# Kernel optimization log

Hardware: AMD Instinct MI355X
Metric: run time of the kernel (lower is better)

The kernel has to match this reference:

```python
import jax, jax.numpy as jnp
import numpy as np

EPS = 1e-5

def _layernorm(x, g, b):
    mu = jnp.mean(x, axis=-1, keepdims=True)
    var = jnp.mean(jnp.square(x - mu), axis=-1, keepdims=True)
    return (x - mu) * jax.lax.rsqrt(var + EPS) * g + b

def setup_inputs() -> dict:
    key = jax.random.key(0)
    ks = jax.random.split(key, 8)
    B, T, D, H = 2, 2048, 1024, 16
    hd = D // H
    s = 0.02
    return {
        "x": jax.random.normal(ks[0], (B, T, D), jnp.float32),
        "wq": jax.random.normal(ks[1], (H, D, hd), jnp.float32) * s,
        "wk": jax.random.normal(ks[2], (H, D, hd), jnp.float32) * s,
        "wv": jax.random.normal(ks[3], (H, D, hd), jnp.float32) * s,
        "w_proj": jax.random.normal(ks[4], (D, D), jnp.float32) * s,
        "b_proj": jnp.zeros((D,), jnp.float32),
        "w_ff1": jax.random.normal(ks[5], (D, 4 * D), jnp.float32) * s,
        "b_ff1": jnp.zeros((4 * D,), jnp.float32),
        "w_ff2": jax.random.normal(ks[6], (4 * D, D), jnp.float32) * s,
        "b_ff2": jnp.zeros((D,), jnp.float32),
        "ln1_g": jnp.ones((D,), jnp.float32),
        "ln1_b": jnp.zeros((D,), jnp.float32),
        "ln2_g": jnp.ones((D,), jnp.float32),
        "ln2_b": jnp.zeros((D,), jnp.float32),
    }

def reference(x, wq, wk, wv, w_proj, b_proj, w_ff1, b_ff1, w_ff2, b_ff2,
              ln1_g, ln1_b, ln2_g, ln2_b):
    B, T, D = x.shape
    H, _, hd = wq.shape
    # --- self-attention sublayer (pre-LN) ---
    h = _layernorm(x, ln1_g, ln1_b)
    # per-head Q/K/V projections batched over heads (math identical to per-head linears)
    q = jnp.einsum('btd,hds->bhts', h, wq)
    k = jnp.einsum('btd,hds->bhts', h, wk)
    v = jnp.einsum('btd,hds->bhts', h, wv)
    att = jnp.einsum('bhts,bhTs->bhtT', q, k) * (hd ** -0.5)  # [B,H,T,T]
    causal = jnp.tril(jnp.ones((T, T), dtype=bool))
    att = jnp.where(causal, att, jnp.float32(-jnp.inf))
    att = jax.nn.softmax(att, axis=-1)
    o = jnp.einsum('bhtT,bhTs->bhts', att, v)                 # [B,H,T,hd]
    o = o.transpose(0, 2, 1, 3).reshape(B, T, H * hd)         # concat heads
    x = x + o @ w_proj + b_proj
    # --- FFN sublayer (pre-LN) ---
    h2 = _layernorm(x, ln2_g, ln2_b)
    ff = jax.nn.relu(h2 @ w_ff1 + b_ff1) @ w_ff2 + b_ff2
    return x + ff
```

## Files before the change

### kernel.cpp

```cpp
#include <hip/hip_runtime.h>

typedef unsigned short u16;
typedef unsigned int   u32;
typedef __bf16 bf16;
typedef bf16 bf16x8 __attribute__((ext_vector_type(8)));
typedef float f32x4 __attribute__((ext_vector_type(4)));
typedef u32 u32x4 __attribute__((ext_vector_type(4)));

__device__ inline u16 f2bf(float f) {
  union { float f; u32 u; } cv; cv.f = f;
  u32 u = cv.u;
  return (u16)((u + 0x7FFFu + ((u >> 16) & 1u)) >> 16);
}

__device__ __forceinline__ void gld16(const void* g, void* l) {
  __builtin_amdgcn_global_load_lds(
      (const __attribute__((address_space(1))) void*)g,
      (__attribute__((address_space(3))) void*)l, 16, 0, 0);
}

template<bool ADDB>
__global__ __launch_bounds__(256) void ln_kernel(
    const float* __restrict__ x, const float* __restrict__ g,
    const float* __restrict__ b, u16* __restrict__ out,
    const float* __restrict__ badd, float* __restrict__ xwb)
{
  const int row = blockIdx.x;
  const int t = threadIdx.x;
  const float4 v = *reinterpret_cast<const float4*>(&x[(size_t)row*1024 + t*4]);
  float s  = v.x + v.y + v.z + v.w;
  float sq = v.x*v.x + v.y*v.y + v.z*v.z + v.w*v.w;
  #pragma unroll
  for (int off = 32; off; off >>= 1) { s += __shfl_down(s, off); sq += __shfl_down(sq, off); }
  __shared__ float red[8];
  const int wave = t >> 6, lane = t & 63;
  if (lane == 0) { red[wave] = s; red[wave + 4] = sq; }
  __syncthreads();
  __shared__ float stats[2];
  if (t == 0) {
    float S  = red[0] + red[1] + red[2] + red[3];
    float SQ = red[4] + red[5] + red[6] + red[7];
    float mu = S * (1.0f/1024.0f);
    float var = SQ * (1.0f/1024.0f) - mu*mu;
    stats[0] = mu; stats[1] = rsqrtf(var + 1e-5f);
  }
  __syncthreads();
  const float mu = stats[0], rv = stats[1];
  const float4 gv = *reinterpret_cast<const float4*>(&g[t*4]);
  const float4 bv = *reinterpret_cast<const float4*>(&b[t*4]);
  u16 o4[4];
  o4[0] = f2bf((v.x - mu)*rv*gv.x + bv.x);
  o4[1] = f2bf((v.y - mu)*rv*gv.y + bv.y);
  o4[2] = f2bf((v.z - mu)*rv*gv.z + bv.z);
  o4[3] = f2bf((v.w - mu)*rv*gv.w + bv.w);
  u32 p0 = (u32)o4[0] | ((u32)o4[1] << 16);
  u32 p1 = (u32)o4[2] | ((u32)o4[3] << 16);
  u32* op = reinterpret_cast<u32*>(&out[(size_t)row*1024 + t*4]);
  op[0] = p0; op[1] = p1;
  if (ADDB) {
    const float4 av = *reinterpret_cast<const float4*>(&badd[t*4]);
    float4 w;
    w.x = v.x + av.x; w.y = v.y + av.y; w.z = v.z + av.z; w.w = v.w + av.w;
    *reinterpret_cast<float4*>(&xwb[(size_t)row*1024 + t*4]) = w;
  }
}

__global__ __launch_bounds__(256) void transpose_cast(
    const float* __restrict__ in, u16* __restrict__ out, int R, int C)
{
  __shared__ float tile[32][33];
  const int tx = threadIdx.x, ty = threadIdx.y;
  const size_t bo = (size_t)blockIdx.z * R * C;
  const int r0 = blockIdx.y * 32, c0 = blockIdx.x * 32;
  #pragma unroll
  for (int j = 0; j < 4; ++j)
    tile[ty + j*8][tx] = in[bo + (size_t)(r0 + ty + j*8)*C + c0 + tx];
  __syncthreads();
  #pragma unroll
  for (int j = 0; j < 4; ++j)
    out[bo + (size_t)(c0 + ty + j*8)*R + r0 + tx] = f2bf(tile[tx][ty + j*8]);
}

__global__ __launch_bounds__(256) void vt_kernel(
    const u16* __restrict__ qkv, u16* __restrict__ vt, int T)
{
  __shared__ u16 tile[32][33];
  const int tx = threadIdx.x, ty = threadIdx.y;
  const int bh = blockIdx.z, b = bh >> 4, h = bh & 15;
  const int r0 = blockIdx.x * 32;
  const int c0 = blockIdx.y * 32;
  const size_t tokbase = (size_t)b * T;
  #pragma unroll
  for (int j = 0; j < 4; ++j)
    tile[ty + j*8][tx] = qkv[(tokbase + r0 + ty + j*8)*3072 + 2048 + h*64 + c0 + tx];
  __syncthreads();
  #pragma unroll
  for (int j = 0; j < 4; ++j)
    vt[((size_t)bh*64 + c0 + ty + j*8)*T + r0 + tx] = tile[tx][ty + j*8];
}

__global__ __launch_bounds__(512, 2) void gemm_128(
    const u16* __restrict__ A, const u16* __restrict__ BT,
    int M, int N, int K,
    const float* __restrict__ bias, const float* __restrict__ resid,
    float* __restrict__ Cout)
{
  __shared__ __align__(16) u16 Alds[2][128*64];
  __shared__ __align__(16) u16 Blds[2][128*64];
  const int t = threadIdx.x;
  const int wave = t >> 6, lane = t & 63;
  const int wm = wave >> 2, wn = wave & 3;
  const int g = lane >> 4, r = lane & 15;
  const int m0 = blockIdx.y * 128, n0 = blockIdx.x * 128;
  const int NTk = K >> 6;

  f32x4 acc[4][2] = {};

  auto STAGE = [&](int buf, int kt) {
    const int k0 = kt << 6;
    #pragma unroll
    for (int p = 0; p < 2; ++p) {
      const int c = t + p*512;
      const int row = c >> 3;
      const int col = (((c & 7) ^ (row & 7)) << 3);
      gld16(&A[(size_t)(m0 + row)*K + k0 + col], &Alds[buf][c*8]);
    }
    #pragma unroll
    for (int p = 0; p < 2; ++p) {
      const int c = t + p*512;
      const int row = c >> 3;
      const int col = (((c & 7) ^ (row & 7)) << 3);
      gld16(&BT[(size_t)(n0 + row)*K + k0 + col], &Blds[buf][c*8]);
    }
  };

  STAGE(0, 0);
  if (NTk > 1) STAGE(1, 1);

  const int csw = (r & 7) << 3;

  for (int kt = 0; kt < NTk; ++kt) {
    const int buf = kt & 1;
    if (kt + 1 < NTk) asm volatile("s_waitcnt vmcnt(4)" ::: "memory");
    else              asm volatile("s_waitcnt vmcnt(0)" ::: "memory");
    __builtin_amdgcn_s_barrier();
    #pragma unroll
    for (int ks = 0; ks < 2; ++ks) {
      bf16x8 af[4], bfr[2];
      #pragma unroll
      for (int i = 0; i < 4; ++i)
        af[i] = *reinterpret_cast<const bf16x8*>(
            &Alds[buf][(wm*64 + i*16 + r)*64 + ((ks*32 + g*8) ^ csw)]);
      #pragma unroll
      for (int j = 0; j < 2; ++j)
        bfr[j] = *reinterpret_cast<const bf16x8*>(
            &Blds[buf][(wn*32 + j*16 + r)*64 + ((ks*32 + g*8) ^ csw)]);
      __builtin_amdgcn_s_setprio(1);
      #pragma unroll
      for (int i = 0; i < 4; ++i)
        #pragma unroll
        for (int j = 0; j < 2; ++j)
          acc[i][j] = __builtin_amdgcn_mfma_f32_16x16x32_bf16(af[i], bfr[j], acc[i][j], 0, 0, 0);
      __builtin_amdgcn_s_setprio(0);
    }
    __builtin_amdgcn_s_barrier();
    if (kt + 2 < NTk) STAGE(buf, kt + 2);
  }

  #pragma unroll
  for (int mi = 0; mi < 4; ++mi) {
    #pragma unroll
    for (int ni = 0; ni < 2; ++ni) {
      #pragma unroll
      for (int i = 0; i < 4; ++i) {
        const int gm = m0 + wm*64 + mi*16 + g*4 + i;
        const int gn = n0 + wn*32 + ni*16 + r;
        const size_t idx = (size_t)gm * N + gn;
        Cout[idx] = acc[mi][ni][i] + bias[gn] + resid[idx];
      }
    }
  }
}

__global__ __launch_bounds__(512, 2) void gemm_128_sk(
    const u16* __restrict__ A, const u16* __restrict__ BT,
    int M, int N, int K, float* __restrict__ Cout)
{
  __shared__ __align__(16) u16 Alds[2][128*64];
  __shared__ __align__(16) u16 Blds[2][128*64];
  const int bid = blockIdx.x;
  const int s = bid >> 3;
  const int n0 = (s & 7) * 128;
  const int m0 = (((s >> 3) & 3) * 8 + (bid & 7)) * 128;
  const int kbase = (s >> 5) * (K >> 1);
  const int t = threadIdx.x;
  const int wave = t >> 6, lane = t & 63;
  const int wm = wave >> 2, wn = wave & 3;
  const int g = lane >> 4, r = lane & 15;
  const int NTk = K >> 7;

  f32x4 acc[4][2] = {};

  auto STAGE = [&](int buf, int kt) {
    const int k0 = kbase + (kt << 6);
    #pragma unroll
    for (int p = 0; p < 2; ++p) {
      const int c = t + p*512;
      const int row = c >> 3;
      const int col = (((c & 7) ^ (row & 7)) << 3);
      gld16(&A[(size_t)(m0 + row)*K + k0 + col], &Alds[buf][c*8]);
    }
    #pragma unroll
    for (int p = 0; p < 2; ++p) {
      const int c = t + p*512;
      const int row = c >> 3;
      const int col = (((c & 7) ^ (row & 7)) << 3);
      gld16(&BT[(size_t)(n0 + row)*K + k0 + col], &Blds[buf][c*8]);
    }
  };

  STAGE(0, 0);
  if (NTk > 1) STAGE(1, 1);

  const int csw = (r & 7) << 3;

  for (int kt = 0; kt < NTk; ++kt) {
    const int buf = kt & 1;
    if (kt + 1 < NTk) asm volatile("s_waitcnt vmcnt(4)" ::: "memory");
    else              asm volatile("s_waitcnt vmcnt(0)" ::: "memory");
    __builtin_amdgcn_s_barrier();
    #pragma unroll
    for (int ks = 0; ks < 2; ++ks) {
      bf16x8 af[4], bfr[2];
      #pragma unroll
      for (int i = 0; i < 4; ++i)
        af[i] = *reinterpret_cast<const bf16x8*>(
            &Alds[buf][(wm*64 + i*16 + r)*64 + ((ks*32 + g*8) ^ csw)]);
      #pragma unroll
      for (int j = 0; j < 2; ++j)
        bfr[j] = *reinterpret_cast<const bf16x8*>(
            &Blds[buf][(wn*32 + j*16 + r)*64 + ((ks*32 + g*8) ^ csw)]);
      __builtin_amdgcn_s_setprio(1);
      #pragma unroll
      for (int i = 0; i < 4; ++i)
        #pragma unroll
        for (int j = 0; j < 2; ++j)
          acc[i][j] = __builtin_amdgcn_mfma_f32_16x16x32_bf16(af[i], bfr[j], acc[i][j], 0, 0, 0);
      __builtin_amdgcn_s_setprio(0);
    }
    __builtin_amdgcn_s_barrier();
    if (kt + 2 < NTk) STAGE(buf, kt + 2);
  }

  #pragma unroll
  for (int mi = 0; mi < 4; ++mi) {
    #pragma unroll
    for (int ni = 0; ni < 2; ++ni) {
      #pragma unroll
      for (int i = 0; i < 4; ++i) {
        const int gm = m0 + wm*64 + mi*16 + g*4 + i;
        const int gn = n0 + wn*32 + ni*16 + r;
        unsafeAtomicAdd(&Cout[(size_t)gm * N + gn], acc[mi][ni][i]);
      }
    }
  }
}

template<int EPI>
__global__ __launch_bounds__(512, 2) void gemm_bt8(
    const u16* __restrict__ A, const u16* __restrict__ BT,
    int M, int N, int K,
    const float* __restrict__ bias, void* __restrict__ Cout)
{
  __shared__ __align__(16) u16 Alds[2][256*64];
  __shared__ __align__(16) u16 Blds[2][256*64];
  const int t = threadIdx.x;
  const int wave = t >> 6, lane = t & 63;
  const int wm = wave >> 2, wn = wave & 3;
  const int g = lane >> 4, r = lane & 15;
  const int m0 = blockIdx.y * 256, n0 = blockIdx.x * 256;
  const int NTk = K >> 6;

  f32x4 acc[8][4] = {};

  auto STAGE = [&](int buf, int kt) {
    const int k0 = kt << 6;
    #pragma unroll
    for (int p = 0; p < 4; ++p) {
      const int c = t + p*512;
      const int row = c >> 3;
      const int col = (((c & 7) ^ (row & 7)) << 3);
      gld16(&A[(size_t)(m0 + row)*K + k0 + col], &Alds[buf][c*8]);
    }
    #pragma unroll
    for (int p = 0; p < 4; ++p) {
      const int c = t + p*512;
      const int row = c >> 3;
      const int col = (((c & 7) ^ (row & 7)) << 3);
      gld16(&BT[(size_t)(n0 + row)*K + k0 + col], &Blds[buf][c*8]);
    }
  };

  STAGE(0, 0);
  if (NTk > 1) STAGE(1, 1);

  const int csw = (r & 7) << 3;

  for (int kt = 0; kt < NTk; ++kt) {
    const int buf = kt & 1;
    if (kt + 1 < NTk) asm volatile("s_waitcnt vmcnt(8)" ::: "memory");
    else              asm volatile("s_waitcnt vmcnt(0)" ::: "memory");
    __builtin_amdgcn_s_barrier();
    #pragma unroll
    for (int p = 0; p < 4; ++p) {
      const int ks = p >> 1, mih = p & 1;
      bf16x8 af[4], bfr[4];
      #pragma unroll
      for (int i = 0; i < 4; ++i) {
        af[i] = *reinterpret_cast<const bf16x8*>(
            &Alds[buf][(wm*128 + (mih*4 + i)*16 + r)*64 + ((ks*32 + g*8) ^ csw)]);
        bfr[i] = *reinterpret_cast<const bf16x8*>(
            &Blds[buf][(wn*64 + i*16 + r)*64 + ((ks*32 + g*8) ^ csw)]);
      }
      __builtin_amdgcn_s_setprio(1);
      #pragma unroll
      for (int i = 0; i < 4; ++i)
        #pragma unroll
        for (int j = 0; j < 4; ++j)
          acc[mih*4 + i][j] =
              __builtin_amdgcn_mfma_f32_16x16x32_bf16(af[i], bfr[j], acc[mih*4 + i][j], 0, 0, 0);
      __builtin_amdgcn_s_setprio(0);
      __builtin_amdgcn_s_barrier();
    }
    if (kt + 2 < NTk) STAGE(buf, kt + 2);
  }

  #pragma unroll
  for (int mi = 0; mi < 8; ++mi) {
    #pragma unroll
    for (int ni = 0; ni < 4; ++ni) {
      #pragma unroll
      for (int i = 0; i < 4; ++i) {
        const int gm = m0 + wm*128 + mi*16 + g*4 + i;
        const int gn = n0 + wn*64 + ni*16 + r;
        const size_t idx = (size_t)gm * N + gn;
        float v = acc[mi][ni][i] + bias[gn];
        ((u16*)Cout)[idx] = f2bf(v > 0.f ? v : 0.f);
      }
    }
  }
}

__global__ __launch_bounds__(512, 2) void gemm_qkv(
    const u16* __restrict__ A, const u16* __restrict__ BT,
    int M, int N, int K, u16* __restrict__ Cout)
{
  __shared__ __align__(16) u16 Alds[2][256*64];
  __shared__ __align__(16) u16 Blds[2][192*64];
  const int t = threadIdx.x;
  const int wave = t >> 6, lane = t & 63;
  const int wm = wave >> 2, wn = wave & 3;
  const int g = lane >> 4, r = lane & 15;
  const int m0 = blockIdx.y * 256, n0 = blockIdx.x * 192;
  const int NTk = K >> 6;

  f32x4 acc[8][3] = {};

  auto STAGE = [&](int buf, int kt) {
    const int k0 = kt << 6;
    #pragma unroll
    for (int p = 0; p < 4; ++p) {
      const int c = t + p*512;
      const int row = c >> 3;
      const int col = (((c & 7) ^ (row & 7)) << 3);
      gld16(&A[(size_t)(m0 + row)*K + k0 + col], &Alds[buf][c*8]);
    }
    #pragma unroll
    for (int p = 0; p < 3; ++p) {
      const int c = t + p*512;
      const int row = c >> 3;
      const int col = (((c & 7) ^ (row & 7)) << 3);
      gld16(&BT[(size_t)(n0 + row)*K + k0 + col], &Blds[buf][c*8]);
    }
  };

  STAGE(0, 0);
  if (NTk > 1) STAGE(1, 1);

  const int csw = (r & 7) << 3;

  for (int kt = 0; kt < NTk; ++kt) {
    const int buf = kt & 1;
    if (kt + 1 < NTk) asm volatile("s_waitcnt vmcnt(7)" ::: "memory");
    else              asm volatile("s_waitcnt vmcnt(0)" ::: "memory");
    __builtin_amdgcn_s_barrier();
    #pragma unroll
    for (int p = 0; p < 4; ++p) {
      const int ks = p >> 1, mih = p & 1;
      bf16x8 af[4], bfr[3];
      #pragma unroll
      for (int i = 0; i < 4; ++i)
        af[i] = *reinterpret_cast<const bf16x8*>(
            &Alds[buf][(wm*128 + (mih*4 + i)*16 + r)*64 + ((ks*32 + g*8) ^ csw)]);
      #pragma unroll
      for (int j = 0; j < 3; ++j)
        bfr[j] = *reinterpret_cast<const bf16x8*>(
            &Blds[buf][(wn*48 + j*16 + r)*64 + ((ks*32 + g*8) ^ csw)]);
      __builtin_amdgcn_s_setprio(1);
      #pragma unroll
      for (int i = 0; i < 4; ++i)
        #pragma unroll
        for (int j = 0; j < 3; ++j)
          acc[mih*4 + i][j] =
              __builtin_amdgcn_mfma_f32_16x16x32_bf16(af[i], bfr[j], acc[mih*4 + i][j], 0, 0, 0);
      __builtin_amdgcn_s_setprio(0);
      __builtin_amdgcn_s_barrier();
    }
    if (kt + 2 < NTk) STAGE(buf, kt + 2);
  }

  #pragma unroll
  for (int mi = 0; mi < 8; ++mi) {
    #pragma unroll
    for (int ni = 0; ni < 3; ++ni) {
      #pragma unroll
      for (int i = 0; i < 4; ++i) {
        const int gm = m0 + wm*128 + mi*16 + g*4 + i;
        const int gn = n0 + wn*48 + ni*16 + r;
        const float sc = (gn < 1024) ? 0.18033688011112042f : 1.0f;
        Cout[(size_t)gm * N + gn] = f2bf(acc[mi][ni][i] * sc);
      }
    }
  }
}

__global__ __launch_bounds__(256, 4) void attn_kernel(
    const u16* __restrict__ qkv, const u16* __restrict__ vt,
    u16* __restrict__ o, int T)
{
  const int bid = blockIdx.x;
  const int bh  = ((bid & 7) << 2) | ((bid >> 3) & 3);
  const int qb  = bid >> 5;
  const int b = bh >> 4, h = bh & 15;
  const int t = threadIdx.x;
  const int wave = t >> 6, lane = t & 63;
  const int g = lane >> 4, r = lane & 15;
  const size_t tokbase = (size_t)b * T;

  __shared__ __align__(16) u16 Klds[2][64*64];
  __shared__ __align__(16) u16 Vlds[2][64*64];
  __shared__ __align__(16) u16 P[4][16*64];

  bf16x8 ones;
  #pragma unroll
  for (int i = 0; i < 8; ++i) ones[i] = (bf16)1.0f;

  auto STAGE = [&](int buf, int kb) {
    const int kv0 = kb*64;
    #pragma unroll
    for (int p = 0; p < 2; ++p) {
      const int c2 = t + p*256;
      const int row = c2 >> 3;
      const int scol = ((c2 & 7) ^ (row & 7)) << 3;
      gld16(&qkv[(tokbase + kv0 + row)*3072 + 1024 + h*64 + scol], &Klds[buf][c2*8]);
      gld16(&vt[((size_t)bh*64 + row)*T + kv0 + scol], &Vlds[buf][c2*8]);
    }
  };

  #pragma unroll 1
  for (int ph = 0; ph < 2; ++ph) {
    const int qa = ph ? qb : (31 - qb);
    const int q0 = qa*64 + wave*16;
    if (ph) __syncthreads();

    bf16x8 qf[2];
    #pragma unroll
    for (int ks = 0; ks < 2; ++ks)
      qf[ks] = *reinterpret_cast<const bf16x8*>(
          &qkv[(tokbase + q0 + r)*3072 + h*64 + ks*32 + g*8]);

    f32x4 acc_o[4] = {};
    f32x4 acc_l = {};
    const int nkv = qa + 1;

    STAGE(0, 0);
    int cur = 0;
    for (int kb = 0; kb < nkv; ++kb) {
      __builtin_amdgcn_s_barrier();
      if (kb + 1 < nkv) {
        STAGE(cur ^ 1, kb + 1);
        asm volatile("s_waitcnt vmcnt(4)" ::: "memory");
      } else {
        asm volatile("s_waitcnt vmcnt(0)" ::: "memory");
      }
      __builtin_amdgcn_s_barrier();
      const int kv0 = kb*64;
      const bool diag = (kb == qa);
      const int cb = (r & 7) << 3;

      f32x4 s[4] = {};
      #pragma unroll
      for (int nb = 0; nb < 4; ++nb) {
        #pragma unroll
        for (int ks = 0; ks < 2; ++ks) {
          bf16x8 kf = *reinterpret_cast<const bf16x8*>(
              &Klds[cur][(nb*16 + r)*64 + ((ks*32 + g*8) ^ cb)]);
          s[nb] = __builtin_amdgcn_mfma_f32_16x16x32_bf16(qf[ks], kf, s[nb], 0, 0, 0);
        }
      }
      #pragma unroll
      for (int i = 0; i < 4; ++i) {
        const int prow = g*4 + i;
        const int pcb = (prow & 7) << 3;
        #pragma unroll
        for (int nb = 0; nb < 4; ++nb) {
          float pv = __builtin_amdgcn_exp2f(s[nb][i]);
          if (diag && (kv0 + nb*16 + r > q0 + prow)) pv = 0.f;
          const bf16 bv = (bf16)pv;
          P[wave][prow*64 + ((nb*16 + r) ^ pcb)] = __builtin_bit_cast(u16, bv);
        }
      }
      #pragma unroll
      for (int ks = 0; ks < 2; ++ks) {
        bf16x8 pf = *reinterpret_cast<const bf16x8*>(
            &P[wave][r*64 + ((ks*32 + g*8) ^ cb)]);
        acc_l = __builtin_amdgcn_mfma_f32_16x16x32_bf16(pf, ones, acc_l, 0, 0, 0);
        #pragma unroll
        for (int nt = 0; nt < 4; ++nt) {
          bf16x8 vf = *reinterpret_cast<const bf16x8*>(
              &Vlds[cur][(nt*16 + r)*64 + ((ks*32 + g*8) ^ cb)]);
          acc_o[nt] = __builtin_amdgcn_mfma_f32_16x16x32_bf16(pf, vf, acc_o[nt], 0, 0, 0);
        }
      }
      cur ^= 1;
    }
    #pragma unroll
    for (int i = 0; i < 4; ++i) {
      const float inv = 1.0f / acc_l[i];
      const size_t rowo = (tokbase + q0 + g*4 + i) * 1024;
      #pragma unroll
      for (int nt = 0; nt < 4; ++nt) {
        const bf16 bv = (bf16)(acc_o[nt][i] * inv);
        o[rowo + h*64 + nt*16 + r] = __builtin_bit_cast(u16, bv);
      }
    }
  }
}

extern "C" void kernel_launch(void* const* d_in, const int* in_sizes, int n_in,
                              void* d_out, int out_size, void* d_ws, size_t ws_size,
                              hipStream_t stream)
{
  const float* x      = (const float*)d_in[0];
  const float* wq     = (const float*)d_in[1];
  const float* wk     = (const float*)d_in[2];
  const float* wv     = (const float*)d_in[3];
  const float* w_proj = (const float*)d_in[4];
  const float* b_proj = (const float*)d_in[5];
  const float* w_ff1  = (const float*)d_in[6];
  const float* b_ff1  = (const float*)d_in[7];
  const float* w_ff2  = (const float*)d_in[8];
  const float* b_ff2  = (const float*)d_in[9];
  const float* ln1_g  = (const float*)d_in[10];
  const float* ln1_b  = (const float*)d_in[11];
  const float* ln2_g  = (const float*)d_in[12];
  const float* ln2_b  = (const float*)d_in[13];

  const int T = 2048;
  const int NT = 4096;

  char* ws = (char*)d_ws;
  u16* Wbuf   = (u16*)(ws);
  u16* hbuf   = (u16*)(ws + ((size_t)8  << 20));
  u16* qkvbuf = (u16*)(ws + ((size_t)16 << 20));
  u16* obuf   = (u16*)(ws + ((size_t)40 << 20));
  u16* ff1buf = qkvbuf;
  u16* vtbuf  = Wbuf;
  float* x1   = (float*)d_out;

  ln_kernel<false><<<dim3(NT), dim3(256), 0, stream>>>(x, ln1_g, ln1_b, hbuf, nullptr, nullptr);
  transpose_cast<<<dim3(2, 32, 16), dim3(32, 8), 0, stream>>>(wq, Wbuf + 0*1024*1024, 1024, 64);
  transpose_cast<<<dim3(2, 32, 16), dim3(32, 8), 0, stream>>>(wk, Wbuf + 1*1024*1024, 1024, 64);
  transpose_cast<<<dim3(2, 32, 16), dim3(32, 8), 0, stream>>>(wv, Wbuf + 2*1024*1024, 1024, 64);
  gemm_qkv<<<dim3(16, 16), dim3(512), 0, stream>>>(hbuf, Wbuf, NT, 3072, 1024, qkvbuf);
  vt_kernel<<<dim3(64, 2, 32), dim3(32, 8), 0, stream>>>(qkvbuf, vtbuf, T);
  attn_kernel<<<dim3(512), dim3(256), 0, stream>>>(qkvbuf, vtbuf, obuf, T);
  transpose_cast<<<dim3(32, 32, 1), dim3(32, 8), 0, stream>>>(w_proj, Wbuf, 1024, 1024);
  gemm_128<<<dim3(8, 32), dim3(512), 0, stream>>>(obuf, Wbuf, NT, 1024, 1024, b_proj, x, x1);
  ln_kernel<true><<<dim3(NT), dim3(256), 0, stream>>>(x1, ln2_g, ln2_b, hbuf, b_ff2, x1);
  transpose_cast<<<dim3(128, 32, 1), dim3(32, 8), 0, stream>>>(w_ff1, Wbuf, 1024, 4096);
  gemm_bt8<2><<<dim3(16, 16), dim3(512), 0, stream>>>(hbuf, Wbuf, NT, 4096, 1024, b_ff1, ff1buf);
  transpose_cast<<<dim3(32, 128, 1), dim3(32, 8), 0, stream>>>(w_ff2, Wbuf, 4096, 1024);
  gemm_128_sk<<<dim3(512), dim3(512), 0, stream>>>(ff1buf, Wbuf, NT, 1024, 4096, (float*)d_out);
}
```

Baseline: 238.5 us.

## Split long causal attention rows across two blocks with atomic partial merge

The attention grid grows from 512 to 1024 blocks. Each long query block's KV range is split so that half 0 handles the first 17 KV tiles and half 1 handles the rest, followed by the short query block. Partial unnormalized outputs and row sums for the upper 1024 query rows are accumulated with float atomics into a scratch area in the output buffer. A new normalization kernel then divides and writes them as bf16. This aims for more parallelism and better load balance, at the cost of a memset, atomic traffic and an extra kernel launch.

```diff
diff --git a/kernel.cpp b/kernel.cpp
--- a/kernel.cpp
+++ b/kernel.cpp
@@ -436,11 +436,15 @@
 
 __global__ __launch_bounds__(256, 4) void attn_kernel(
     const u16* __restrict__ qkv, const u16* __restrict__ vt,
-    u16* __restrict__ o, int T)
+    u16* __restrict__ o, float* __restrict__ opart,
+    float* __restrict__ lpart, int T)
 {
   const int bid = blockIdx.x;
-  const int bh  = ((bid & 7) << 2) | ((bid >> 3) & 3);
-  const int qb  = bid >> 5;
+  const int half = bid >> 9;
+  const int idx = bid & 511;
+  const int bh  = ((idx & 7) << 2) | ((idx >> 3) & 3);
+  const int qb  = idx >> 5;
+  const int qL = 31 - qb, qS = qb;
   const int b = bh >> 4, h = bh & 15;
   const int t = threadIdx.x;
   const int wave = t >> 6, lane = t & 63;
@@ -455,8 +459,8 @@
   #pragma unroll
   for (int i = 0; i < 8; ++i) ones[i] = (bf16)1.0f;
 
-  auto STAGE = [&](int buf, int kb) {
-    const int kv0 = kb*64;
+  auto STAGE = [&](int buf, int kbg) {
+    const int kv0 = kbg*64;
     #pragma unroll
     for (int p = 0; p < 2; ++p) {
       const int c2 = t + p*256;
@@ -467,11 +471,20 @@
     }
   };
 
+  int seg_qa[2], seg_kv0[2], seg_cnt[2], nseg = 0;
+  bool seg_at[2];
+  if (half == 0) {
+    seg_qa[0] = qL; seg_kv0[0] = 0; seg_cnt[0] = 17; seg_at[0] = true; nseg = 1;
+  } else {
+    if (qb < 15) { seg_qa[0] = qL; seg_kv0[0] = 17; seg_cnt[0] = 15 - qb; seg_at[0] = true; nseg = 1; }
+    seg_qa[nseg] = qS; seg_kv0[nseg] = 0; seg_cnt[nseg] = qb + 1; seg_at[nseg] = false; ++nseg;
+  }
+
   #pragma unroll 1
-  for (int ph = 0; ph < 2; ++ph) {
-    const int qa = ph ? qb : (31 - qb);
+  for (int sgi = 0; sgi < nseg; ++sgi) {
+    const int qa = seg_qa[sgi], kvb = seg_kv0[sgi], nkv = seg_cnt[sgi];
     const int q0 = qa*64 + wave*16;
-    if (ph) __syncthreads();
+    if (sgi) __syncthreads();
 
     bf16x8 qf[2];
     #pragma unroll
@@ -481,21 +494,21 @@
 
     f32x4 acc_o[4] = {};
     f32x4 acc_l = {};
-    const int nkv = qa + 1;
-
-    STAGE(0, 0);
+
+    STAGE(0, kvb);
     int cur = 0;
     for (int kb = 0; kb < nkv; ++kb) {
       __builtin_amdgcn_s_barrier();
       if (kb + 1 < nkv) {
-        STAGE(cur ^ 1, kb + 1);
+        STAGE(cur ^ 1, kvb + kb + 1);
         asm volatile("s_waitcnt vmcnt(4)" ::: "memory");
       } else {
         asm volatile("s_waitcnt vmcnt(0)" ::: "memory");
       }
       __builtin_amdgcn_s_barrier();
-      const int kv0 = kb*64;
-      const bool diag = (kb == qa);
+      const int kbg = kvb + kb;
+      const int kv0 = kbg*64;
+      const bool diag = (kbg == qa);
       const int cb = (r & 7) << 3;
 
       f32x4 s[4] = {};
@@ -534,17 +547,53 @@
       }
       cur ^= 1;
     }
-    #pragma unroll
-    for (int i = 0; i < 4; ++i) {
-      const float inv = 1.0f / acc_l[i];
-      const size_t rowo = (tokbase + q0 + g*4 + i) * 1024;
-      #pragma unroll
-      for (int nt = 0; nt < 4; ++nt) {
-        const bf16 bv = (bf16)(acc_o[nt][i] * inv);
-        o[rowo + h*64 + nt*16 + r] = __builtin_bit_cast(u16, bv);
-      }
-    }
-  }
+
+    if (seg_at[sgi]) {
+      #pragma unroll
+      for (int i = 0; i < 4; ++i) {
+        const int rloc = q0 + g*4 + i - 1024;
+        #pragma unroll
+        for (int nt = 0; nt < 4; ++nt)
+          unsafeAtomicAdd(&opart[((size_t)(b*1024 + rloc))*1024 + h*64 + nt*16 + r],
+                          acc_o[nt][i]);
+        if (r == 0)
+          unsafeAtomicAdd(&lpart[(b*16 + h)*1024 + rloc], acc_l[i]);
+      }
+    } else {
+      #pragma unroll
+      for (int i = 0; i < 4; ++i) {
+        const float inv = 1.0f / acc_l[i];
+        const size_t rowo = (tokbase + q0 + g*4 + i) * 1024;
+        #pragma unroll
+        for (int nt = 0; nt < 4; ++nt) {
+          const bf16 bv = (bf16)(acc_o[nt][i] * inv);
+          o[rowo + h*64 + nt*16 + r] = __builtin_bit_cast(u16, bv);
+        }
+      }
+    }
+  }
+}
+
+__global__ __launch_bounds__(256) void attn_norm(
+    const float* __restrict__ opart, const float* __restrict__ lpart,
+    u16* __restrict__ o, int T)
+{
+  const int bid = blockIdx.x;
+  const int b = bid >> 10, rloc = bid & 1023;
+  const int t = threadIdx.x;
+  const float4 v = *reinterpret_cast<const float4*>(
+      &opart[((size_t)(b*1024 + rloc))*1024 + t*4]);
+  const int h = t >> 4;
+  const float inv = 1.0f / lpart[(b*16 + h)*1024 + rloc];
+  u16 o4[4];
+  o4[0] = __builtin_bit_cast(u16, (bf16)(v.x * inv));
+  o4[1] = __builtin_bit_cast(u16, (bf16)(v.y * inv));
+  o4[2] = __builtin_bit_cast(u16, (bf16)(v.z * inv));
+  o4[3] = __builtin_bit_cast(u16, (bf16)(v.w * inv));
+  u32 p0 = (u32)o4[0] | ((u32)o4[1] << 16);
+  u32 p1 = (u32)o4[2] | ((u32)o4[3] << 16);
+  u32* op = reinterpret_cast<u32*>(&o[((size_t)(b*T + 1024 + rloc))*1024 + t*4]);
+  op[0] = p0; op[1] = p1;
 }
 
 extern "C" void kernel_launch(void* const* d_in, const int* in_sizes, int n_in,
@@ -577,14 +626,18 @@
   u16* ff1buf = qkvbuf;
   u16* vtbuf  = Wbuf;
   float* x1   = (float*)d_out;
-
+  float* opart = (float*)d_out;
+  float* lpart = (float*)((char*)d_out + ((size_t)8 << 20));
+
+  hipMemsetAsync(d_out, 0, ((size_t)8 << 20) + 32*1024*4, stream);
   ln_kernel<false><<<dim3(NT), dim3(256), 0, stream>>>(x, ln1_g, ln1_b, hbuf, nullptr, nullptr);
   transpose_cast<<<dim3(2, 32, 16), dim3(32, 8), 0, stream>>>(wq, Wbuf + 0*1024*1024, 1024, 64);
   transpose_cast<<<dim3(2, 32, 16), dim3(32, 8), 0, stream>>>(wk, Wbuf + 1*1024*1024, 1024, 64);
   transpose_cast<<<dim3(2, 32, 16), dim3(32, 8), 0, stream>>>(wv, Wbuf + 2*1024*1024, 1024, 64);
   gemm_qkv<<<dim3(16, 16), dim3(512), 0, stream>>>(hbuf, Wbuf, NT, 3072, 1024, qkvbuf);
   vt_kernel<<<dim3(64, 2, 32), dim3(32, 8), 0, stream>>>(qkvbuf, vtbuf, T);
-  attn_kernel<<<dim3(512), dim3(256), 0, stream>>>(qkvbuf, vtbuf, obuf, T);
+  attn_kernel<<<dim3(1024), dim3(256), 0, stream>>>(qkvbuf, vtbuf, obuf, opart, lpart, T);
+  attn_norm<<<dim3(2048), dim3(256), 0, stream>>>(opart, lpart, obuf, T);
   transpose_cast<<<dim3(32, 32, 1), dim3(32, 8), 0, stream>>>(w_proj, Wbuf, 1024, 1024);
   gemm_128<<<dim3(8, 32), dim3(512), 0, stream>>>(obuf, Wbuf, NT, 1024, 1024, b_proj, x, x1);
   ln_kernel<true><<<dim3(NT), dim3(256), 0, stream>>>(x1, ln2_g, ln2_b, hbuf, b_ff2, x1);
```

Measured after the change: 251.7 us. 5.5% more time.
